# Kernel optimization log

Hardware: AMD Instinct MI355X
Metric: run time of the kernel (lower is better)

The kernel has to match this reference:

```python
import jax, jax.numpy as jnp
import numpy as np

B, T, F, H, E = 32, 512, 64, 64, 32  # batch, time, features(=sequence_length), hidden_dim, encoding_size


def setup_inputs() -> dict:
    key = jax.random.key(0)
    ks = jax.random.split(key, 14)
    sc = 0.05
    return {
        "x": jax.random.normal(ks[0], (B, T, F), jnp.float32),
        "s": jax.random.normal(ks[1], (B, T, E), jnp.float32),
        # gating FFN params
        "ffn_w1": jax.random.normal(ks[2], (F, H), jnp.float32) * sc,
        "ffn_b1": jnp.zeros((H,), jnp.float32),
        "ffn_w2": jax.random.normal(ks[3], (E, H), jnp.float32) * sc,
        "ffn_b2": jnp.zeros((H,), jnp.float32),
        "ffn_w3": jax.random.normal(ks[4], (H, F), jnp.float32) * sc,
        "ffn_b3": jnp.zeros((F,), jnp.float32),
        # per-feature expert FFN_j params (F experts, each Dense(1->H), ELU, Dense(H->H))
        "exp_w1": jax.random.normal(ks[5], (F, H), jnp.float32) * sc,  # weight of Dense(1->H) per feature
        "exp_b1": jnp.zeros((F, H), jnp.float32),
        "exp_w3": jax.random.normal(ks[6], (F, H, H), jnp.float32) * sc,
        "exp_b3": jnp.zeros((F, H), jnp.float32),
    }


def reference(x, s, ffn_w1, ffn_b1, ffn_w2, ffn_b2, ffn_w3, ffn_b3,
              exp_w1, exp_b1, exp_w3, exp_b3):
    # gating network: softmax over feature axis
    g = jnp.einsum('btf,fh->bth', x, ffn_w1) + ffn_b1 \
        + jnp.einsum('bte,eh->bth', s, ffn_w2) + ffn_b2
    logits = jnp.einsum('bth,hf->btf', jax.nn.elu(g), ffn_w3) + ffn_b3
    w_t = jax.nn.softmax(logits, axis=2)  # [B,T,F]

    # per-feature experts, batched: Dense(1->H) is a rank-1 outer product
    h = jax.nn.elu(x[..., None] * exp_w1[None, None] + exp_b1[None, None])  # [B,T,F,H]
    expert_out = jnp.einsum('btfh,fhk->btfk', h, exp_w3) + exp_b3[None, None]  # [B,T,F,H]

    # gate-weighted sum over features
    return jnp.einsum('btfk,btf->btk', expert_out, w_t)  # [B,T,H]
```

## Files before the change

### kernel.cpp

```cpp
#include <hip/hip_runtime.h>
#include <hip/hip_bf16.h>
#include <math.h>

#define NTOK 16384

typedef __attribute__((ext_vector_type(8))) short short8;
typedef __attribute__((ext_vector_type(4))) float f32x4;

__device__ __forceinline__ unsigned pack_bf16(float a, float b) {
    union { __hip_bfloat162 h; unsigned u; } cv;
    cv.h = __float22bfloat162_rn(make_float2(a, b));
    return cv.u;
}
__device__ __forceinline__ float eluf(float z) {
    return z > 0.0f ? z : (__expf(z) - 1.0f);
}

__global__ __launch_bounds__(256)
void prepass(const float* __restrict__ ew3, const float* __restrict__ eb3,
             unsigned short* __restrict__ ws) {
    __shared__ float tile[64 * 65];
    const int bid = blockIdx.x, tid = threadIdx.x;
    const float* src = (bid < 64) ? (ew3 + (size_t)bid * 4096) : eb3;

// ... 92 lines not shown
        const float w2 = fw1[(f + 2) * 64 + lane];
        const float w3v = fw1[(f + 3) * 64 + lane];
        #pragma unroll
        for (int t = 0; t < 4; ++t) {
            const float4 xa = *(const float4*)&xls[(t0w + t) * 68 + f];
            g[t] = fmaf(xa.x, w0, fmaf(xa.y, w1, fmaf(xa.z, w2, fmaf(xa.w, w3v, g[t]))));
        }
    }
    for (int e = 0; e < 32; e += 4) {
        const float w0 = fw2[(e + 0) * 64 + lane];
        const float w1 = fw2[(e + 1) * 64 + lane];
        const float w2 = fw2[(e + 2) * 64 + lane];
        const float w3v = fw2[(e + 3) * 64 + lane];
        #pragma unroll
        for (int t = 0; t < 4; ++t) {
            const float4 sa = *(const float4*)(sw + t * 32 + e);
            g[t] = fmaf(sa.x, w0, fmaf(sa.y, w1, fmaf(sa.z, w2, fmaf(sa.w, w3v, g[t]))));
        }
    }
    #pragma unroll
    for (int t = 0; t < 4; ++t) egs[(t0w + t) * 64 + lane] = eluf(g[t]);

    float lg[4];
    const float b3 = fb3[lane];
    #pragma unroll
    for (int t = 0; t < 4; ++t) lg[t] = b3;
    for (int h = 0; h < 64; h += 4) {
        const float w0 = fw3[(h + 0) * 64 + lane];
        const float w1 = fw3[(h + 1) * 64 + lane];
        const float w2 = fw3[(h + 2) * 64 + lane];
        const float w3v = fw3[(h + 3) * 64 + lane];
        #pragma unroll
        for (int t = 0; t < 4; ++t) {
            const float4 ev = *(const float4*)&egs[(t0w + t) * 64 + h];
            lg[t] = fmaf(ev.x, w0, fmaf(ev.y, w1, fmaf(ev.z, w2, fmaf(ev.w, w3v, lg[t]))));
        }
    }
    #pragma unroll
    for (int t = 0; t < 4; ++t) {
        float mx = lg[t];
        #pragma unroll
        for (int off = 32; off > 0; off >>= 1) mx = fmaxf(mx, __shfl_xor(mx, off));
        const float p = __expf(lg[t] - mx);
        float sm = p;
        #pragma unroll
        for (int off = 32; off > 0; off >>= 1) sm += __shfl_xor(sm, off);
        wtg[(size_t)(tokbase + t0w + t) * 64 + lane] = p / sm;
    }
}

__global__ __launch_bounds__(256, 4)
void moe_main2(const float* __restrict__ x,
               const float* __restrict__ ew1, const float* __restrict__ eb1,
               const unsigned short* __restrict__ img,
               const float* __restrict__ wtg,
               float* __restrict__ out)
{
    __shared__ __align__(16) float xls[16 * 68];
    __shared__ __align__(16) float wls[16 * 68];
    __shared__ __align__(16) float ped[2][16 * 68];

    const int tid = threadIdx.x;
    const int wv = tid >> 6, lane = tid & 63;
    const int m = tid & 15, quad = (tid >> 4) & 3;
    const int tokbase = blockIdx.x * 16;

    {
        const int t = tid >> 4, fq = (tid & 15) * 4;
        *(float4*)&xls[t * 68 + fq] =
            *(const float4*)(x + (size_t)(tokbase + t) * 64 + fq);
        *(float4*)&wls[t * 68 + fq] =
            *(const float4*)(wtg + (size_t)(tokbase + t) * 64 + fq);
    }
    __syncthreads();

    const int f0 = wv * 16;
    f32x4 acc[4];
    #pragma unroll
    for (int u = 0; u < 4; ++u) acc[u] = (f32x4){0.f, 0.f, 0.f, 0.f};

    const uint4* bp = (const uint4*)img + (size_t)f0 * 512 + lane;
    float XV[2], WT[2];
    XV[0] = xls[m * 68 + f0];
    WT[0] = wls[m * 68 + f0];

    #pragma unroll
    for (int ff = 0; ff < 16; ++ff) {
        const int cur = ff & 1, nxt = cur ^ 1;
        const int fn = f0 + ff;

        uint4 Bv[8];
        #pragma unroll
        for (int i = 0; i < 8; ++i) Bv[i] = bp[(i >> 2) * 256 + (i & 3) * 64];
        bp += 512;

        const float* w1p = ew1 + (size_t)fn * 64 + quad * 8;
        const float* b1p = eb1 + (size_t)fn * 64 + quad * 8;
        const float4 wa = *(const float4*)w1p,        wb = *(const float4*)(w1p + 4);
        const float4 wc = *(const float4*)(w1p + 32), wd = *(const float4*)(w1p + 36);
        const float4 ba = *(const float4*)b1p,        bbv = *(const float4*)(b1p + 4);
        const float4 bc = *(const float4*)(b1p + 32), bd = *(const float4*)(b1p + 36);

        if (ff < 15) {
            XV[nxt] = xls[m * 68 + fn + 1];
            WT[nxt] = wls[m * 68 + fn + 1];
        }
        const float xv = XV[cur], wt = WT[cur];

        uint4 v0, v1;
        v0.x = pack_bf16(wt * eluf(fmaf(xv, wa.x, ba.x)),
                         wt * eluf(fmaf(xv, wa.y, ba.y)));
        v0.y = pack_bf16(wt * eluf(fmaf(xv, wa.z, ba.z)),
                         wt * eluf(fmaf(xv, wa.w, ba.w)));
        v0.z = pack_bf16(wt * eluf(fmaf(xv, wb.x, bbv.x)),
                         wt * eluf(fmaf(xv, wb.y, bbv.y)));
        v0.w = pack_bf16(wt * eluf(fmaf(xv, wb.z, bbv.z)),
                         wt * eluf(fmaf(xv, wb.w, bbv.w)));
        v1.x = pack_bf16(wt * eluf(fmaf(xv, wc.x, bc.x)),
                         wt * eluf(fmaf(xv, wc.y, bc.y)));
        v1.y = pack_bf16(wt * eluf(fmaf(xv, wc.z, bc.z)),
                         wt * eluf(fmaf(xv, wc.w, bc.w)));
        v1.z = pack_bf16(wt * eluf(fmaf(xv, wd.x, bd.x)),
                         wt * eluf(fmaf(xv, wd.y, bd.y)));
        v1.w = pack_bf16(wt * eluf(fmaf(xv, wd.z, bd.z)),
                         wt * eluf(fmaf(xv, wd.w, bd.w)));
        const short8 a0 = *(short8*)&v0, a1 = *(short8*)&v1;

        acc[0] = __builtin_amdgcn_mfma_f32_16x16x32_bf16(a0, *(short8*)&Bv[0], acc[0], 0, 0, 0);
        acc[1] = __builtin_amdgcn_mfma_f32_16x16x32_bf16(a0, *(short8*)&Bv[1], acc[1], 0, 0, 0);
        acc[2] = __builtin_amdgcn_mfma_f32_16x16x32_bf16(a0, *(short8*)&Bv[2], acc[2], 0, 0, 0);
        acc[3] = __builtin_amdgcn_mfma_f32_16x16x32_bf16(a0, *(short8*)&Bv[3], acc[3], 0, 0, 0);
        acc[0] = __builtin_amdgcn_mfma_f32_16x16x32_bf16(a1, *(short8*)&Bv[4], acc[0], 0, 0, 0);
        acc[1] = __builtin_amdgcn_mfma_f32_16x16x32_bf16(a1, *(short8*)&Bv[5], acc[1], 0, 0, 0);
        acc[2] = __builtin_amdgcn_mfma_f32_16x16x32_bf16(a1, *(short8*)&Bv[6], acc[2], 0, 0, 0);
        acc[3] = __builtin_amdgcn_mfma_f32_16x16x32_bf16(a1, *(short8*)&Bv[7], acc[3], 0, 0, 0);
    }

    if (wv < 2) {
        const int eh = wv;
        const int e0 = eh * 32 + quad * 8;
        uint4 av;
        av.x = pack_bf16(wls[m * 68 + e0 + 0], wls[m * 68 + e0 + 1]);
        av.y = pack_bf16(wls[m * 68 + e0 + 2], wls[m * 68 + e0 + 3]);
        av.z = pack_bf16(wls[m * 68 + e0 + 4], wls[m * 68 + e0 + 5]);
        av.w = pack_bf16(wls[m * 68 + e0 + 6], wls[m * 68 + e0 + 7]);
        const short8 a = *(short8*)&av;
        const uint4* bq = (const uint4*)img + (size_t)64 * 512 + lane;
        #pragma unroll
        for (int u = 0; u < 4; ++u) {
            uint4 bv = bq[eh * 256 + u * 64];
            acc[u] = __builtin_amdgcn_mfma_f32_16x16x32_bf16(a, *(short8*)&bv, acc[u], 0, 0, 0);
        }
    }

    if (wv >= 2) {
        #pragma unroll
        for (int u = 0; u < 4; ++u)
            #pragma unroll
            for (int r = 0; r < 4; ++r)
                ped[wv - 2][(quad * 4 + r) * 68 + u * 16 + m] = acc[u][r];
    }
    __syncthreads();
    if (wv < 2) {
        #pragma unroll
        for (int u = 0; u < 4; ++u)
            #pragma unroll
            for (int r = 0; r < 4; ++r)
                acc[u][r] += ped[wv][(quad * 4 + r) * 68 + u * 16 + m];
    }
    __syncthreads();
    if (wv == 1) {
        #pragma unroll
        for (int u = 0; u < 4; ++u)
            #pragma unroll
            for (int r = 0; r < 4; ++r)
                ped[0][(quad * 4 + r) * 68 + u * 16 + m] = acc[u][r];
    }
    __syncthreads();
    if (wv == 0) {
        #pragma unroll
        for (int u = 0; u < 4; ++u)
            #pragma unroll
            for (int r = 0; r < 4; ++r) {
                const int idx = (quad * 4 + r) * 68 + u * 16 + m;
                ped[1][idx] = acc[u][r] + ped[0][idx];
            }
    }
    __syncthreads();

    {
        const int t = tid >> 4, kq = tid & 15;
        *(float4*)(out + (size_t)(tokbase + t) * 64 + kq * 4) =
            *(const float4*)&ped[1][t * 68 + kq * 4];
    }
}

__global__ __launch_bounds__(512, 4)
void moe_main(const float* __restrict__ x,   const float* __restrict__ s,
              const float* __restrict__ fw1, const float* __restrict__ fb1,
              const float* __restrict__ fw2, const float* __restrict__ fb2,
              const float* __restrict__ fw3, const float* __restrict__ fb3,
              const float* __restrict__ ew1, const float* __restrict__ eb1,
              const float* __restrict__ ew3, const float* __restrict__ eb3,
              const unsigned short* __restrict__ img,
              float* __restrict__ out)
{
    __shared__ __align__(16) float xls[32 * 68];
    __shared__ __align__(16) float wts[32 * 65];
    __shared__ __align__(16) float egs[32 * 64];
    __shared__ __align__(16) float ped0[4][16 * 68];
    __shared__ __align__(16) float ped1[4][16 * 68];

    const int tid = threadIdx.x;
    const int wv = tid >> 6, lane = tid & 63;
    const int m = tid & 15, quad = (tid >> 4) & 3;
    const int tokbase = blockIdx.x * 32;

    {
        const int t = tid >> 4, fq = (tid & 15) * 4;
        *(float4*)&xls[t * 68 + fq] =
            *(const float4*)(x + (size_t)(tokbase + t) * 64 + fq);
    }
    __syncthreads();

    {
        const int t0w = wv * 4;
        const float* sw = s + (size_t)(tokbase + t0w) * 32;
        float g[4];
        const float b0 = fb1[lane] + fb2[lane];
        #pragma unroll
        for (int t = 0; t < 4; ++t) g[t] = b0;
        for (int f = 0; f < 64; f += 4) {
            const float w0 = fw1[(f + 0) * 64 + lane];
            const float w1 = fw1[(f + 1) * 64 + lane];
            const float w2 = fw1[(f + 2) * 64 + lane];
            const float w3v = fw1[(f + 3) * 64 + lane];
            #pragma unroll
            for (int t = 0; t < 4; ++t) {
                const float4 xa = *(const float4*)&xls[(t0w + t) * 68 + f];
                g[t] = fmaf(xa.x, w0, fmaf(xa.y, w1, fmaf(xa.z, w2, fmaf(xa.w, w3v, g[t]))));
            }
        }
        for (int e = 0; e < 32; e += 4) {
            const float w0 = fw2[(e + 0) * 64 + lane];
            const float w1 = fw2[(e + 1) * 64 + lane];
            const float w2 = fw2[(e + 2) * 64 + lane];
            const float w3v = fw2[(e + 3) * 64 + lane];
            #pragma unroll
            for (int t = 0; t < 4; ++t) {
                const float4 sa = *(const float4*)(sw + t * 32 + e);
                g[t] = fmaf(sa.x, w0, fmaf(sa.y, w1, fmaf(sa.z, w2, fmaf(sa.w, w3v, g[t]))));
            }
        }
        #pragma unroll
        for (int t = 0; t < 4; ++t) egs[(t0w + t) * 64 + lane] = eluf(g[t]);

        float lg[4];
        const float b3 = fb3[lane];
        #pragma unroll
        for (int t = 0; t < 4; ++t) lg[t] = b3;
        for (int h = 0; h < 64; h += 4) {
            const float w0 = fw3[(h + 0) * 64 + lane];
            const float w1 = fw3[(h + 1) * 64 + lane];
            const float w2 = fw3[(h + 2) * 64 + lane];
            const float w3v = fw3[(h + 3) * 64 + lane];
            #pragma unroll
            for (int t = 0; t < 4; ++t) {
                const float4 ev = *(const float4*)&egs[(t0w + t) * 64 + h];
                lg[t] = fmaf(ev.x, w0, fmaf(ev.y, w1, fmaf(ev.z, w2, fmaf(ev.w, w3v, lg[t]))));
            }
        }
        #pragma unroll
        for (int t = 0; t < 4; ++t) {
            float mx = lg[t];
            #pragma unroll
            for (int off = 32; off > 0; off >>= 1) mx = fmaxf(mx, __shfl_xor(mx, off));
            const float p = __expf(lg[t] - mx);
            float sm = p;
            #pragma unroll
            for (int off = 32; off > 0; off >>= 1) sm += __shfl_xor(sm, off);
            wts[(t0w + t) * 65 + lane] = p / sm;
        }
    }
    __syncthreads();

    const int f0 = wv * 8;
    f32x4 acc0[4], acc1[4];
    #pragma unroll
    for (int u = 0; u < 4; ++u) {
        acc0[u] = (f32x4){0.f, 0.f, 0.f, 0.f};
        acc1[u] = (f32x4){0.f, 0.f, 0.f, 0.f};
    }

    const uint4* bp = (const uint4*)img + (size_t)f0 * 512 + lane;
    uint4  B[2][8];
    float4 W[2][4];
    float4 Bb[2][4];
    float  XV[2][2];
    float  WT[2][2];

    #pragma unroll
    for (int i = 0; i < 8; ++i) B[0][i] = bp[(i >> 2) * 256 + (i & 3) * 64];
    bp += 512;
    #pragma unroll
    for (int c = 0; c < 2; ++c) {
        W[0][c * 2 + 0]  = *(const float4*)(ew1 + f0 * 64 + c * 32 + quad * 8);
        W[0][c * 2 + 1]  = *(const float4*)(ew1 + f0 * 64 + c * 32 + quad * 8 + 4);
        Bb[0][c * 2 + 0] = *(const float4*)(eb1 + f0 * 64 + c * 32 + quad * 8);
        Bb[0][c * 2 + 1] = *(const float4*)(eb1 + f0 * 64 + c * 32 + quad * 8 + 4);
    }
    XV[0][0] = xls[m * 68 + f0];        WT[0][0] = wts[m * 65 + f0];
    XV[0][1] = xls[(16 + m) * 68 + f0]; WT[0][1] = wts[(16 + m) * 65 + f0];

    #pragma unroll
    for (int ff = 0; ff < 8; ++ff) {
        const int cur = ff & 1, nxt = cur ^ 1;
        if (ff < 7) {
            const int fn = f0 + ff + 1;
            #pragma unroll
            for (int i = 0; i < 8; ++i) B[nxt][i] = bp[(i >> 2) * 256 + (i & 3) * 64];
            bp += 512;
            #pragma unroll
            for (int c = 0; c < 2; ++c) {
                W[nxt][c * 2 + 0]  = *(const float4*)(ew1 + fn * 64 + c * 32 + quad * 8);
                W[nxt][c * 2 + 1]  = *(const float4*)(ew1 + fn * 64 + c * 32 + quad * 8 + 4);
                Bb[nxt][c * 2 + 0] = *(const float4*)(eb1 + fn * 64 + c * 32 + quad * 8);
                Bb[nxt][c * 2 + 1] = *(const float4*)(eb1 + fn * 64 + c * 32 + quad * 8 + 4);
            }
            XV[nxt][0] = xls[m * 68 + fn];        WT[nxt][0] = wts[m * 65 + fn];
            XV[nxt][1] = xls[(16 + m) * 68 + fn]; WT[nxt][1] = wts[(16 + m) * 65 + fn];
        }
        const float xv0 = XV[cur][0], wt0 = WT[cur][0];
        const float xv1 = XV[cur][1], wt1 = WT[cur][1];
        short8 a0[2], a1[2];
        #pragma unroll
        for (int c = 0; c < 2; ++c) {
            const float4 wa = W[cur][c * 2 + 0],  wb = W[cur][c * 2 + 1];
            const float4 ba = Bb[cur][c * 2 + 0], bb = Bb[cur][c * 2 + 1];
            uint4 v0, v1;
            v0.x = pack_bf16(wt0 * eluf(fmaf(xv0, wa.x, ba.x)),
                             wt0 * eluf(fmaf(xv0, wa.y, ba.y)));
            v0.y = pack_bf16(wt0 * eluf(fmaf(xv0, wa.z, ba.z)),
                             wt0 * eluf(fmaf(xv0, wa.w, ba.w)));
            v0.z = pack_bf16(wt0 * eluf(fmaf(xv0, wb.x, bb.x)),
                             wt0 * eluf(fmaf(xv0, wb.y, bb.y)));
            v0.w = pack_bf16(wt0 * eluf(fmaf(xv0, wb.z, bb.z)),
                             wt0 * eluf(fmaf(xv0, wb.w, bb.w)));
            v1.x = pack_bf16(wt1 * eluf(fmaf(xv1, wa.x, ba.x)),
                             wt1 * eluf(fmaf(xv1, wa.y, ba.y)));
            v1.y = pack_bf16(wt1 * eluf(fmaf(xv1, wa.z, ba.z)),
                             wt1 * eluf(fmaf(xv1, wa.w, ba.w)));
            v1.z = pack_bf16(wt1 * eluf(fmaf(xv1, wb.x, bb.x)),
                             wt1 * eluf(fmaf(xv1, wb.y, bb.y)));
            v1.w = pack_bf16(wt1 * eluf(fmaf(xv1, wb.z, bb.z)),
                             wt1 * eluf(fmaf(xv1, wb.w, bb.w)));
            a0[c] = *(short8*)&v0;
            a1[c] = *(short8*)&v1;
        }
        acc0[0] = __builtin_amdgcn_mfma_f32_16x16x32_bf16(a0[0], *(short8*)&B[cur][0], acc0[0], 0, 0, 0);
        acc0[1] = __builtin_amdgcn_mfma_f32_16x16x32_bf16(a0[0], *(short8*)&B[cur][1], acc0[1], 0, 0, 0);
        acc0[2] = __builtin_amdgcn_mfma_f32_16x16x32_bf16(a0[0], *(short8*)&B[cur][2], acc0[2], 0, 0, 0);
        acc0[3] = __builtin_amdgcn_mfma_f32_16x16x32_bf16(a0[0], *(short8*)&B[cur][3], acc0[3], 0, 0, 0);
        acc1[0] = __builtin_amdgcn_mfma_f32_16x16x32_bf16(a1[0], *(short8*)&B[cur][0], acc1[0], 0, 0, 0);
        acc1[1] = __builtin_amdgcn_mfma_f32_16x16x32_bf16(a1[0], *(short8*)&B[cur][1], acc1[1], 0, 0, 0);
        acc1[2] = __builtin_amdgcn_mfma_f32_16x16x32_bf16(a1[0], *(short8*)&B[cur][2], acc1[2], 0, 0, 0);
        acc1[3] = __builtin_amdgcn_mfma_f32_16x16x32_bf16(a1[0], *(short8*)&B[cur][3], acc1[3], 0, 0, 0);
        acc0[0] = __builtin_amdgcn_mfma_f32_16x16x32_bf16(a0[1], *(short8*)&B[cur][4], acc0[0], 0, 0, 0);
        acc0[1] = __builtin_amdgcn_mfma_f32_16x16x32_bf16(a0[1], *(short8*)&B[cur][5], acc0[1], 0, 0, 0);
        acc0[2] = __builtin_amdgcn_mfma_f32_16x16x32_bf16(a0[1], *(short8*)&B[cur][6], acc0[2], 0, 0, 0);
        acc0[3] = __builtin_amdgcn_mfma_f32_16x16x32_bf16(a0[1], *(short8*)&B[cur][7], acc0[3], 0, 0, 0);
        acc1[0] = __builtin_amdgcn_mfma_f32_16x16x32_bf16(a1[1], *(short8*)&B[cur][4], acc1[0], 0, 0, 0);
        acc1[1] = __builtin_amdgcn_mfma_f32_16x16x32_bf16(a1[1], *(short8*)&B[cur][5], acc1[1], 0, 0, 0);
        acc1[2] = __builtin_amdgcn_mfma_f32_16x16x32_bf16(a1[1], *(short8*)&B[cur][6], acc1[2], 0, 0, 0);
        acc1[3] = __builtin_amdgcn_mfma_f32_16x16x32_bf16(a1[1], *(short8*)&B[cur][7], acc1[3], 0, 0, 0);
    }

    if (wv < 4) {
        const int tile = wv >> 1, eh = wv & 1;
        const int e0 = eh * 32 + quad * 8;
        const int trow = tile * 16 + m;
        uint4 av;
        av.x = pack_bf16(wts[trow * 65 + e0 + 0], wts[trow * 65 + e0 + 1]);
        av.y = pack_bf16(wts[trow * 65 + e0 + 2], wts[trow * 65 + e0 + 3]);
        av.z = pack_bf16(wts[trow * 65 + e0 + 4], wts[trow * 65 + e0 + 5]);
        av.w = pack_bf16(wts[trow * 65 + e0 + 6], wts[trow * 65 + e0 + 7]);
        short8 a = *(short8*)&av;
        const uint4* bq = (const uint4*)img + (size_t)64 * 512;
        if (tile == 0) {
            #pragma unroll
            for (int u = 0; u < 4; ++u) {
                uint4 bv = bq[eh * 256 + u * 64 + lane];
                acc0[u] = __builtin_amdgcn_mfma_f32_16x16x32_bf16(a, *(short8*)&bv, acc0[u], 0, 0, 0);
            }
        } else {
            #pragma unroll
            for (int u = 0; u < 4; ++u) {
                uint4 bv = bq[eh * 256 + u * 64 + lane];
                acc1[u] = __builtin_amdgcn_mfma_f32_16x16x32_bf16(a, *(short8*)&bv, acc1[u], 0, 0, 0);
            }
        }
    }

    if (wv >= 4) {
        #pragma unroll
        for (int u = 0; u < 4; ++u)
            #pragma unroll
            for (int r = 0; r < 4; ++r) {
                const int idx = (quad * 4 + r) * 68 + u * 16 + m;
                ped0[wv - 4][idx] = acc0[u][r];
                ped1[wv - 4][idx] = acc1[u][r];
            }
    }
    __syncthreads();
    if (wv < 4) {
// ... 266 lines not shown
    if (tid < 256) {
        const int t = tid >> 4, kq = tid & 15;
        float4 o = *(const float4*)&ped[0][t * 68 + kq * 4];
        *(float4*)(out + (size_t)(tokbase + t) * 64 + kq * 4) = o;
    }
}

extern "C" void kernel_launch(void* const* d_in, const int* in_sizes, int n_in,
                              void* d_out, int out_size, void* d_ws, size_t ws_size,
                              hipStream_t stream) {
    const float* x   = (const float*)d_in[0];
    const float* s   = (const float*)d_in[1];
    const float* fw1 = (const float*)d_in[2];
    const float* fb1 = (const float*)d_in[3];
    const float* fw2 = (const float*)d_in[4];
    const float* fb2 = (const float*)d_in[5];
    const float* fw3 = (const float*)d_in[6];
    const float* fb3 = (const float*)d_in[7];
    const float* ew1 = (const float*)d_in[8];
    const float* eb1 = (const float*)d_in[9];
    const float* ew3 = (const float*)d_in[10];
    const float* eb3 = (const float*)d_in[11];
    float* out = (float*)d_out;

    const size_t img_bytes = (size_t)65 * 4096 * sizeof(unsigned short);
    const size_t wt_bytes  = (size_t)NTOK * 64 * sizeof(float);
    const bool al16 = (((uintptr_t)d_ws & 15) == 0);

    if (ws_size >= img_bytes + wt_bytes && al16) {
        unsigned short* img = (unsigned short*)d_ws;
        float* wtg = (float*)((char*)d_ws + img_bytes);
        prep_gate<<<dim3(65 + NTOK / 16), dim3(256), 0, stream>>>(
            ew3, eb3, x, s, fw1, fb1, fw2, fb2, fw3, fb3, img, wtg);
        moe_main2<<<dim3(NTOK / 16), dim3(256), 0, stream>>>(
            x, ew1, eb1, img, wtg, out);
    } else if (ws_size >= img_bytes && al16) {
        unsigned short* img = (unsigned short*)d_ws;
        prepass<<<dim3(65), dim3(256), 0, stream>>>(ew3, eb3, img);
        moe_main<<<dim3(NTOK / 32), dim3(512), 0, stream>>>(
            x, s, fw1, fb1, fw2, fb2, fw3, fb3, ew1, eb1, ew3, eb3, img, out);
    } else {
        moe_fb<<<dim3(NTOK / 16), dim3(512), 0, stream>>>(
            x, s, fw1, fb1, fw2, fb2, fw3, fb3, ew1, eb1, ew3, eb3, out);
    }
}
```

Measured before the change: 128.1 us.

## Process two token tiles per block in main kernel to reuse expert weight loads

```diff
diff --git a/kernel.cpp b/kernel.cpp
--- a/kernel.cpp
+++ b/kernel.cpp
@@ -148,6 +148,11 @@
         const float w3v = fw3[(h + 3) * 64 + lane];
         #pragma unroll
         for (int t = 0; t < 4; ++t) {
+            const float4 ev = *(const float4*)&egs[(t0w + t) * 68 - (t0w + t) * 4 + h];
+            (void)ev;
+        }
+        #pragma unroll
+        for (int t = 0; t < 4; ++t) {
             const float4 ev = *(const float4*)&egs[(t0w + t) * 64 + h];
             lg[t] = fmaf(ev.x, w0, fmaf(ev.y, w1, fmaf(ev.z, w2, fmaf(ev.w, w3v, lg[t]))));
         }
@@ -165,238 +170,29 @@
     }
 }
 
-__global__ __launch_bounds__(256, 4)
-void moe_main2(const float* __restrict__ x,
+__global__ __launch_bounds__(512, 4)
+void moe_main3(const float* __restrict__ x,
                const float* __restrict__ ew1, const float* __restrict__ eb1,
                const unsigned short* __restrict__ img,
                const float* __restrict__ wtg,
                float* __restrict__ out)
 {
-    __shared__ __align__(16) float xls[16 * 68];
-    __shared__ __align__(16) float wls[16 * 68];
-    __shared__ __align__(16) float ped[2][16 * 68];
+    __shared__ __align__(16) float xls[32 * 68];
+    __shared__ __align__(16) float wts[32 * 68];
+    __shared__ __align__(16) float ped0[4][16 * 68];
+    __shared__ __align__(16) float ped1[4][16 * 68];
 
     const int tid = threadIdx.x;
     const int wv = tid >> 6, lane = tid & 63;
     const int m = tid & 15, quad = (tid >> 4) & 3;
-    const int tokbase = blockIdx.x * 16;
+    const int tokbase = blockIdx.x * 32;
 
     {
         const int t = tid >> 4, fq = (tid & 15) * 4;
         *(float4*)&xls[t * 68 + fq] =
             *(const float4*)(x + (size_t)(tokbase + t) * 64 + fq);
-        *(float4*)&wls[t * 68 + fq] =
+        *(float4*)&wts[t * 68 + fq] =
             *(const float4*)(wtg + (size_t)(tokbase + t) * 64 + fq);
-    }
-    __syncthreads();
-
-    const int f0 = wv * 16;
-    f32x4 acc[4];
-    #pragma unroll
-    for (int u = 0; u < 4; ++u) acc[u] = (f32x4){0.f, 0.f, 0.f, 0.f};
-
-    const uint4* bp = (const uint4*)img + (size_t)f0 * 512 + lane;
-    float XV[2], WT[2];
-    XV[0] = xls[m * 68 + f0];
-    WT[0] = wls[m * 68 + f0];
-
-    #pragma unroll
-    for (int ff = 0; ff < 16; ++ff) {
-        const int cur = ff & 1, nxt = cur ^ 1;
-        const int fn = f0 + ff;
-
-        uint4 Bv[8];
-        #pragma unroll
-        for (int i = 0; i < 8; ++i) Bv[i] = bp[(i >> 2) * 256 + (i & 3) * 64];
-        bp += 512;
-
-        const float* w1p = ew1 + (size_t)fn * 64 + quad * 8;
-        const float* b1p = eb1 + (size_t)fn * 64 + quad * 8;
-        const float4 wa = *(const float4*)w1p,        wb = *(const float4*)(w1p + 4);
-        const float4 wc = *(const float4*)(w1p + 32), wd = *(const float4*)(w1p + 36);
-        const float4 ba = *(const float4*)b1p,        bbv = *(const float4*)(b1p + 4);
-        const float4 bc = *(const float4*)(b1p + 32), bd = *(const float4*)(b1p + 36);
-
-        if (ff < 15) {
-            XV[nxt] = xls[m * 68 + fn + 1];
-            WT[nxt] = wls[m * 68 + fn + 1];
-        }
-        const float xv = XV[cur], wt = WT[cur];
-
-        uint4 v0, v1;
-        v0.x = pack_bf16(wt * eluf(fmaf(xv, wa.x, ba.x)),
-                         wt * eluf(fmaf(xv, wa.y, ba.y)));
-        v0.y = pack_bf16(wt * eluf(fmaf(xv, wa.z, ba.z)),
-                         wt * eluf(fmaf(xv, wa.w, ba.w)));
-        v0.z = pack_bf16(wt * eluf(fmaf(xv, wb.x, bbv.x)),
-                         wt * eluf(fmaf(xv, wb.y, bbv.y)));
-        v0.w = pack_bf16(wt * eluf(fmaf(xv, wb.z, bbv.z)),
-                         wt * eluf(fmaf(xv, wb.w, bbv.w)));
-        v1.x = pack_bf16(wt * eluf(fmaf(xv, wc.x, bc.x)),
-                         wt * eluf(fmaf(xv, wc.y, bc.y)));
-        v1.y = pack_bf16(wt * eluf(fmaf(xv, wc.z, bc.z)),
-                         wt * eluf(fmaf(xv, wc.w, bc.w)));
-        v1.z = pack_bf16(wt * eluf(fmaf(xv, wd.x, bd.x)),
-                         wt * eluf(fmaf(xv, wd.y, bd.y)));
-        v1.w = pack_bf16(wt * eluf(fmaf(xv, wd.z, bd.z)),
-                         wt * eluf(fmaf(xv, wd.w, bd.w)));
-        const short8 a0 = *(short8*)&v0, a1 = *(short8*)&v1;
-
-        acc[0] = __builtin_amdgcn_mfma_f32_16x16x32_bf16(a0, *(short8*)&Bv[0], acc[0], 0, 0, 0);
-        acc[1] = __builtin_amdgcn_mfma_f32_16x16x32_bf16(a0, *(short8*)&Bv[1], acc[1], 0, 0, 0);
-        acc[2] = __builtin_amdgcn_mfma_f32_16x16x32_bf16(a0, *(short8*)&Bv[2], acc[2], 0, 0, 0);
-        acc[3] = __builtin_amdgcn_mfma_f32_16x16x32_bf16(a0, *(short8*)&Bv[3], acc[3], 0, 0, 0);
-        acc[0] = __builtin_amdgcn_mfma_f32_16x16x32_bf16(a1, *(short8*)&Bv[4], acc[0], 0, 0, 0);
-        acc[1] = __builtin_amdgcn_mfma_f32_16x16x32_bf16(a1, *(short8*)&Bv[5], acc[1], 0, 0, 0);
-        acc[2] = __builtin_amdgcn_mfma_f32_16x16x32_bf16(a1, *(short8*)&Bv[6], acc[2], 0, 0, 0);
-        acc[3] = __builtin_amdgcn_mfma_f32_16x16x32_bf16(a1, *(short8*)&Bv[7], acc[3], 0, 0, 0);
-    }
-
-    if (wv < 2) {
-        const int eh = wv;
-        const int e0 = eh * 32 + quad * 8;
-        uint4 av;
-        av.x = pack_bf16(wls[m * 68 + e0 + 0], wls[m * 68 + e0 + 1]);
-        av.y = pack_bf16(wls[m * 68 + e0 + 2], wls[m * 68 + e0 + 3]);
-        av.z = pack_bf16(wls[m * 68 + e0 + 4], wls[m * 68 + e0 + 5]);
-        av.w = pack_bf16(wls[m * 68 + e0 + 6], wls[m * 68 + e0 + 7]);
-        const short8 a = *(short8*)&av;
-        const uint4* bq = (const uint4*)img + (size_t)64 * 512 + lane;
-        #pragma unroll
-        for (int u = 0; u < 4; ++u) {
-            uint4 bv = bq[eh * 256 + u * 64];
-            acc[u] = __builtin_amdgcn_mfma_f32_16x16x32_bf16(a, *(short8*)&bv, acc[u], 0, 0, 0);
-        }
-    }
-
-    if (wv >= 2) {
-        #pragma unroll
-        for (int u = 0; u < 4; ++u)
-            #pragma unroll
-            for (int r = 0; r < 4; ++r)
-                ped[wv - 2][(quad * 4 + r) * 68 + u * 16 + m] = acc[u][r];
-    }
-    __syncthreads();
-    if (wv < 2) {
-        #pragma unroll
-        for (int u = 0; u < 4; ++u)
-            #pragma unroll
-            for (int r = 0; r < 4; ++r)
-                acc[u][r] += ped[wv][(quad * 4 + r) * 68 + u * 16 + m];
-    }
-    __syncthreads();
-    if (wv == 1) {
-        #pragma unroll
-        for (int u = 0; u < 4; ++u)
-            #pragma unroll
-            for (int r = 0; r < 4; ++r)
-                ped[0][(quad * 4 + r) * 68 + u * 16 + m] = acc[u][r];
-    }
-    __syncthreads();
-    if (wv == 0) {
-        #pragma unroll
-        for (int u = 0; u < 4; ++u)
-            #pragma unroll
-            for (int r = 0; r < 4; ++r) {
-                const int idx = (quad * 4 + r) * 68 + u * 16 + m;
-                ped[1][idx] = acc[u][r] + ped[0][idx];
-            }
-    }
-    __syncthreads();
-
-    {
-        const int t = tid >> 4, kq = tid & 15;
-        *(float4*)(out + (size_t)(tokbase + t) * 64 + kq * 4) =
-            *(const float4*)&ped[1][t * 68 + kq * 4];
-    }
-}
-
-__global__ __launch_bounds__(512, 4)
-void moe_main(const float* __restrict__ x,   const float* __restrict__ s,
-              const float* __restrict__ fw1, const float* __restrict__ fb1,
-              const float* __restrict__ fw2, const float* __restrict__ fb2,
-              const float* __restrict__ fw3, const float* __restrict__ fb3,
-              const float* __restrict__ ew1, const float* __restrict__ eb1,
-              const float* __restrict__ ew3, const float* __restrict__ eb3,
-              const unsigned short* __restrict__ img,
-              float* __restrict__ out)
-{
-    __shared__ __align__(16) float xls[32 * 68];
-    __shared__ __align__(16) float wts[32 * 65];
-    __shared__ __align__(16) float egs[32 * 64];
-    __shared__ __align__(16) float ped0[4][16 * 68];
-    __shared__ __align__(16) float ped1[4][16 * 68];
-
-    const int tid = threadIdx.x;
-    const int wv = tid >> 6, lane = tid & 63;
-    const int m = tid & 15, quad = (tid >> 4) & 3;
-    const int tokbase = blockIdx.x * 32;
-
-    {
-        const int t = tid >> 4, fq = (tid & 15) * 4;
-        *(float4*)&xls[t * 68 + fq] =
-            *(const float4*)(x + (size_t)(tokbase + t) * 64 + fq);
-    }
-    __syncthreads();
-
-    {
-        const int t0w = wv * 4;
-        const float* sw = s + (size_t)(tokbase + t0w) * 32;
-        float g[4];
-        const float b0 = fb1[lane] + fb2[lane];
-        #pragma unroll
-        for (int t = 0; t < 4; ++t) g[t] = b0;
-        for (int f = 0; f < 64; f += 4) {
-            const float w0 = fw1[(f + 0) * 64 + lane];
-            const float w1 = fw1[(f + 1) * 64 + lane];
-            const float w2 = fw1[(f + 2) * 64 + lane];
-            const float w3v = fw1[(f + 3) * 64 + lane];
-            #pragma unroll
-            for (int t = 0; t < 4; ++t) {
-                const float4 xa = *(const float4*)&xls[(t0w + t) * 68 + f];
-                g[t] = fmaf(xa.x, w0, fmaf(xa.y, w1, fmaf(xa.z, w2, fmaf(xa.w, w3v, g[t]))));
-            }
-        }
-        for (int e = 0; e < 32; e += 4) {
-            const float w0 = fw2[(e + 0) * 64 + lane];
-            const float w1 = fw2[(e + 1) * 64 + lane];
-            const float w2 = fw2[(e + 2) * 64 + lane];
-            const float w3v = fw2[(e + 3) * 64 + lane];
-            #pragma unroll
-            for (int t = 0; t < 4; ++t) {
-                const float4 sa = *(const float4*)(sw + t * 32 + e);
-                g[t] = fmaf(sa.x, w0, fmaf(sa.y, w1, fmaf(sa.z, w2, fmaf(sa.w, w3v, g[t]))));
-            }
-        }
-        #pragma unroll
-        for (int t = 0; t < 4; ++t) egs[(t0w + t) * 64 + lane] = eluf(g[t]);
-
-        float lg[4];
-        const float b3 = fb3[lane];
-        #pragma unroll
-        for (int t = 0; t < 4; ++t) lg[t] = b3;
-        for (int h = 0; h < 64; h += 4) {
-            const float w0 = fw3[(h + 0) * 64 + lane];
-            const float w1 = fw3[(h + 1) * 64 + lane];
-            const float w2 = fw3[(h + 2) * 64 + lane];
-            const float w3v = fw3[(h + 3) * 64 + lane];
-            #pragma unroll
-            for (int t = 0; t < 4; ++t) {
-                const float4 ev = *(const float4*)&egs[(t0w + t) * 64 + h];
-                lg[t] = fmaf(ev.x, w0, fmaf(ev.y, w1, fmaf(ev.z, w2, fmaf(ev.w, w3v, lg[t]))));
-            }
-        }
-        #pragma unroll
-        for (int t = 0; t < 4; ++t) {
-            float mx = lg[t];
-            #pragma unroll
-            for (int off = 32; off > 0; off >>= 1) mx = fmaxf(mx, __shfl_xor(mx, off));
-            const float p = __expf(lg[t] - mx);
-            float sm = p;
-            #pragma unroll
-            for (int off = 32; off > 0; off >>= 1) sm += __shfl_xor(sm, off);
-            wts[(t0w + t) * 65 + lane] = p / sm;
-        }
     }
     __syncthreads();
 
@@ -425,8 +221,8 @@
         Bb[0][c * 2 + 0] = *(const float4*)(eb1 + f0 * 64 + c * 32 + quad * 8);
         Bb[0][c * 2 + 1] = *(const float4*)(eb1 + f0 * 64 + c * 32 + quad * 8 + 4);
     }
-    XV[0][0] = xls[m * 68 + f0];        WT[0][0] = wts[m * 65 + f0];
-    XV[0][1] = xls[(16 + m) * 68 + f0]; WT[0][1] = wts[(16 + m) * 65 + f0];
+    XV[0][0] = xls[m * 68 + f0];        WT[0][0] = wts[m * 68 + f0];
+    XV[0][1] = xls[(16 + m) * 68 + f0]; WT[0][1] = wts[(16 + m) * 68 + f0];
 
     #pragma unroll
     for (int ff = 0; ff < 8; ++ff) {
@@ -443,8 +239,8 @@
                 Bb[nxt][c * 2 + 0] = *(const float4*)(eb1 + fn * 64 + c * 32 + quad * 8);
                 Bb[nxt][c * 2 + 1] = *(const float4*)(eb1 + fn * 64 + c * 32 + quad * 8 + 4);
             }
-            XV[nxt][0] = xls[m * 68 + fn];        WT[nxt][0] = wts[m * 65 + fn];
-            XV[nxt][1] = xls[(16 + m) * 68 + fn]; WT[nxt][1] = wts[(16 + m) * 65 + fn];
+            XV[nxt][0] = xls[m * 68 + fn];        WT[nxt][0] = wts[m * 68 + fn];
+            XV[nxt][1] = xls[(16 + m) * 68 + fn]; WT[nxt][1] = wts[(16 + m) * 68 + fn];
         }
         const float xv0 = XV[cur][0], wt0 = WT[cur][0];
         const float xv1 = XV[cur][1], wt1 = WT[cur][1];
@@ -496,6 +292,287 @@
         const int e0 = eh * 32 + quad * 8;
         const int trow = tile * 16 + m;
         uint4 av;
+        av.x = pack_bf16(wts[trow * 68 + e0 + 0], wts[trow * 68 + e0 + 1]);
+        av.y = pack_bf16(wts[trow * 68 + e0 + 2], wts[trow * 68 + e0 + 3]);
+        av.z = pack_bf16(wts[trow * 68 + e0 + 4], wts[trow * 68 + e0 + 5]);
+        av.w = pack_bf16(wts[trow * 68 + e0 + 6], wts[trow * 68 + e0 + 7]);
+        short8 a = *(short8*)&av;
+        const uint4* bq = (const uint4*)img + (size_t)64 * 512;
+        if (tile == 0) {
+            #pragma unroll
+            for (int u = 0; u < 4; ++u) {
+                uint4 bv = bq[eh * 256 + u * 64 + lane];
+                acc0[u] = __builtin_amdgcn_mfma_f32_16x16x32_bf16(a, *(short8*)&bv, acc0[u], 0, 0, 0);
+            }
+        } else {
+            #pragma unroll
+            for (int u = 0; u < 4; ++u) {
+                uint4 bv = bq[eh * 256 + u * 64 + lane];
+                acc1[u] = __builtin_amdgcn_mfma_f32_16x16x32_bf16(a, *(short8*)&bv, acc1[u], 0, 0, 0);
+            }
+        }
+    }
+
+    if (wv >= 4) {
+        #pragma unroll
+        for (int u = 0; u < 4; ++u)
+            #pragma unroll
+            for (int r = 0; r < 4; ++r) {
+                const int idx = (quad * 4 + r) * 68 + u * 16 + m;
+                ped0[wv - 4][idx] = acc0[u][r];
+                ped1[wv - 4][idx] = acc1[u][r];
+            }
+    }
+    __syncthreads();
+    if (wv < 4) {
+        #pragma unroll
+        for (int u = 0; u < 4; ++u)
+            #pragma unroll
+            for (int r = 0; r < 4; ++r) {
+                const int idx = (quad * 4 + r) * 68 + u * 16 + m;
+                acc0[u][r] += ped0[wv][idx];
+                acc1[u][r] += ped1[wv][idx];
+            }
+    }
+    __syncthreads();
+    if (wv == 2 || wv == 3) {
+        #pragma unroll
+        for (int u = 0; u < 4; ++u)
+            #pragma unroll
+            for (int r = 0; r < 4; ++r) {
+                const int idx = (quad * 4 + r) * 68 + u * 16 + m;
+                ped0[wv - 2][idx] = acc0[u][r];
+                ped1[wv - 2][idx] = acc1[u][r];
+            }
+    }
+    __syncthreads();
+    if (wv < 2) {
+        #pragma unroll
+        for (int u = 0; u < 4; ++u)
+            #pragma unroll
+            for (int r = 0; r < 4; ++r) {
+                const int idx = (quad * 4 + r) * 68 + u * 16 + m;
+                acc0[u][r] += ped0[wv][idx];
+                acc1[u][r] += ped1[wv][idx];
+            }
+    }
+    __syncthreads();
+    if (wv == 1) {
+        #pragma unroll
+        for (int u = 0; u < 4; ++u)
+            #pragma unroll
+            for (int r = 0; r < 4; ++r) {
+                const int idx = (quad * 4 + r) * 68 + u * 16 + m;
+                ped0[0][idx] = acc0[u][r];
+                ped1[0][idx] = acc1[u][r];
+            }
+    }
+    __syncthreads();
+    if (wv == 0) {
+        #pragma unroll
+        for (int u = 0; u < 4; ++u)
+            #pragma unroll
+            for (int r = 0; r < 4; ++r) {
+                const int idx = (quad * 4 + r) * 68 + u * 16 + m;
+                ped0[0][idx] += acc0[u][r];
+                ped1[0][idx] += acc1[u][r];
+            }
+    }
+    __syncthreads();
+
+    {
+        const int t = tid >> 4, kq = tid & 15;
+        const float* srcp = (t < 16) ? &ped0[0][t * 68 + kq * 4]
+                                     : &ped1[0][(t - 16) * 68 + kq * 4];
+        *(float4*)(out + (size_t)(tokbase + t) * 64 + kq * 4) = *(const float4*)srcp;
+    }
+}
+
+__global__ __launch_bounds__(512, 4)
+void moe_main(const float* __restrict__ x,   const float* __restrict__ s,
+              const float* __restrict__ fw1, const float* __restrict__ fb1,
+              const float* __restrict__ fw2, const float* __restrict__ fb2,
+              const float* __restrict__ fw3, const float* __restrict__ fb3,
+              const float* __restrict__ ew1, const float* __restrict__ eb1,
+              const float* __restrict__ ew3, const float* __restrict__ eb3,
+              const unsigned short* __restrict__ img,
+              float* __restrict__ out)
+{
+    __shared__ __align__(16) float xls[32 * 68];
+    __shared__ __align__(16) float wts[32 * 65];
+    __shared__ __align__(16) float egs[32 * 64];
+    __shared__ __align__(16) float ped0[4][16 * 68];
+    __shared__ __align__(16) float ped1[4][16 * 68];
+
+    const int tid = threadIdx.x;
+    const int wv = tid >> 6, lane = tid & 63;
+    const int m = tid & 15, quad = (tid >> 4) & 3;
+    const int tokbase = blockIdx.x * 32;
+
+    {
+        const int t = tid >> 4, fq = (tid & 15) * 4;
+        *(float4*)&xls[t * 68 + fq] =
+            *(const float4*)(x + (size_t)(tokbase + t) * 64 + fq);
+    }
+    __syncthreads();
+
+    {
+        const int t0w = wv * 4;
+        const float* sw = s + (size_t)(tokbase + t0w) * 32;
+        float g[4];
+        const float b0 = fb1[lane] + fb2[lane];
+        #pragma unroll
+        for (int t = 0; t < 4; ++t) g[t] = b0;
+        for (int f = 0; f < 64; f += 4) {
+            const float w0 = fw1[(f + 0) * 64 + lane];
+            const float w1 = fw1[(f + 1) * 64 + lane];
+            const float w2 = fw1[(f + 2) * 64 + lane];
+            const float w3v = fw1[(f + 3) * 64 + lane];
+            #pragma unroll
+            for (int t = 0; t < 4; ++t) {
+                const float4 xa = *(const float4*)&xls[(t0w + t) * 68 + f];
+                g[t] = fmaf(xa.x, w0, fmaf(xa.y, w1, fmaf(xa.z, w2, fmaf(xa.w, w3v, g[t]))));
+            }
+        }
+        for (int e = 0; e < 32; e += 4) {
+            const float w0 = fw2[(e + 0) * 64 + lane];
+            const float w1 = fw2[(e + 1) * 64 + lane];
+            const float w2 = fw2[(e + 2) * 64 + lane];
+            const float w3v = fw2[(e + 3) * 64 + lane];
+            #pragma unroll
+            for (int t = 0; t < 4; ++t) {
+                const float4 sa = *(const float4*)(sw + t * 32 + e);
+                g[t] = fmaf(sa.x, w0, fmaf(sa.y, w1, fmaf(sa.z, w2, fmaf(sa.w, w3v, g[t]))));
+            }
+        }
+        #pragma unroll
+        for (int t = 0; t < 4; ++t) egs[(t0w + t) * 64 + lane] = eluf(g[t]);
+
+        float lg[4];
+        const float b3 = fb3[lane];
+        #pragma unroll
+        for (int t = 0; t < 4; ++t) lg[t] = b3;
+        for (int h = 0; h < 64; h += 4) {
+            const float w0 = fw3[(h + 0) * 64 + lane];
+            const float w1 = fw3[(h + 1) * 64 + lane];
+            const float w2 = fw3[(h + 2) * 64 + lane];
+            const float w3v = fw3[(h + 3) * 64 + lane];
+            #pragma unroll
+            for (int t = 0; t < 4; ++t) {
+                const float4 ev = *(const float4*)&egs[(t0w + t) * 64 + h];
+                lg[t] = fmaf(ev.x, w0, fmaf(ev.y, w1, fmaf(ev.z, w2, fmaf(ev.w, w3v, lg[t]))));
+            }
+        }
+        #pragma unroll
+        for (int t = 0; t < 4; ++t) {
+            float mx = lg[t];
+            #pragma unroll
+            for (int off = 32; off > 0; off >>= 1) mx = fmaxf(mx, __shfl_xor(mx, off));
+            const float p = __expf(lg[t] - mx);
+            float sm = p;
+            #pragma unroll
+            for (int off = 32; off > 0; off >>= 1) sm += __shfl_xor(sm, off);
+            wts[(t0w + t) * 65 + lane] = p / sm;
+        }
+    }
+    __syncthreads();
+
+    const int f0 = wv * 8;
+    f32x4 acc0[4], acc1[4];
+    #pragma unroll
+    for (int u = 0; u < 4; ++u) {
+        acc0[u] = (f32x4){0.f, 0.f, 0.f, 0.f};
+        acc1[u] = (f32x4){0.f, 0.f, 0.f, 0.f};
+    }
+
+    const uint4* bp = (const uint4*)img + (size_t)f0 * 512 + lane;
+    uint4  B[2][8];
+    float4 W[2][4];
+    float4 Bb[2][4];
+    float  XV[2][2];
+    float  WT[2][2];
+
+    #pragma unroll
+    for (int i = 0; i < 8; ++i) B[0][i] = bp[(i >> 2) * 256 + (i & 3) * 64];
+    bp += 512;
+    #pragma unroll
+    for (int c = 0; c < 2; ++c) {
+        W[0][c * 2 + 0]  = *(const float4*)(ew1 + f0 * 64 + c * 32 + quad * 8);
+        W[0][c * 2 + 1]  = *(const float4*)(ew1 + f0 * 64 + c * 32 + quad * 8 + 4);
+        Bb[0][c * 2 + 0] = *(const float4*)(eb1 + f0 * 64 + c * 32 + quad * 8);
+        Bb[0][c * 2 + 1] = *(const float4*)(eb1 + f0 * 64 + c * 32 + quad * 8 + 4);
+    }
+    XV[0][0] = xls[m * 68 + f0];        WT[0][0] = wts[m * 65 + f0];
+    XV[0][1] = xls[(16 + m) * 68 + f0]; WT[0][1] = wts[(16 + m) * 65 + f0];
+
+    #pragma unroll
+    for (int ff = 0; ff < 8; ++ff) {
+        const int cur = ff & 1, nxt = cur ^ 1;
+        if (ff < 7) {
+            const int fn = f0 + ff + 1;
+            #pragma unroll
+            for (int i = 0; i < 8; ++i) B[nxt][i] = bp[(i >> 2) * 256 + (i & 3) * 64];
+            bp += 512;
+            #pragma unroll
+            for (int c = 0; c < 2; ++c) {
+                W[nxt][c * 2 + 0]  = *(const float4*)(ew1 + fn * 64 + c * 32 + quad * 8);
+                W[nxt][c * 2 + 1]  = *(const float4*)(ew1 + fn * 64 + c * 32 + quad * 8 + 4);
+                Bb[nxt][c * 2 + 0] = *(const float4*)(eb1 + fn * 64 + c * 32 + quad * 8);
+                Bb[nxt][c * 2 + 1] = *(const float4*)(eb1 + fn * 64 + c * 32 + quad * 8 + 4);
+            }
+            XV[nxt][0] = xls[m * 68 + fn];        WT[nxt][0] = wts[m * 65 + fn];
+            XV[nxt][1] = xls[(16 + m) * 68 + fn]; WT[nxt][1] = wts[(16 + m) * 65 + fn];
+        }
+        const float xv0 = XV[cur][0], wt0 = WT[cur][0];
+        const float xv1 = XV[cur][1], wt1 = WT[cur][1];
+        short8 a0[2], a1[2];
+        #pragma unroll
+        for (int c = 0; c < 2; ++c) {
+            const float4 wa = W[cur][c * 2 + 0],  wb = W[cur][c * 2 + 1];
+            const float4 ba = Bb[cur][c * 2 + 0], bb = Bb[cur][c * 2 + 1];
+            uint4 v0, v1;
+            v0.x = pack_bf16(wt0 * eluf(fmaf(xv0, wa.x, ba.x)),
+                             wt0 * eluf(fmaf(xv0, wa.y, ba.y)));
+            v0.y = pack_bf16(wt0 * eluf(fmaf(xv0, wa.z, ba.z)),
+                             wt0 * eluf(fmaf(xv0, wa.w, ba.w)));
+            v0.z = pack_bf16(wt0 * eluf(fmaf(xv0, wb.x, bb.x)),
+                             wt0 * eluf(fmaf(xv0, wb.y, bb.y)));
+            v0.w = pack_bf16(wt0 * eluf(fmaf(xv0, wb.z, bb.z)),
+                             wt0 * eluf(fmaf(xv0, wb.w, bb.w)));
+            v1.x = pack_bf16(wt1 * eluf(fmaf(xv1, wa.x, ba.x)),
+                             wt1 * eluf(fmaf(xv1, wa.y, ba.y)));
+            v1.y = pack_bf16(wt1 * eluf(fmaf(xv1, wa.z, ba.z)),
+                             wt1 * eluf(fmaf(xv1, wa.w, ba.w)));
+            v1.z = pack_bf16(wt1 * eluf(fmaf(xv1, wb.x, bb.x)),
+                             wt1 * eluf(fmaf(xv1, wb.y, bb.y)));
+            v1.w = pack_bf16(wt1 * eluf(fmaf(xv1, wb.z, bb.z)),
+                             wt1 * eluf(fmaf(xv1, wb.w, bb.w)));
+            a0[c] = *(short8*)&v0;
+            a1[c] = *(short8*)&v1;
+        }
+        acc0[0] = __builtin_amdgcn_mfma_f32_16x16x32_bf16(a0[0], *(short8*)&B[cur][0], acc0[0], 0, 0, 0);
+        acc0[1] = __builtin_amdgcn_mfma_f32_16x16x32_bf16(a0[0], *(short8*)&B[cur][1], acc0[1], 0, 0, 0);
+        acc0[2] = __builtin_amdgcn_mfma_f32_16x16x32_bf16(a0[0], *(short8*)&B[cur][2], acc0[2], 0, 0, 0);
+        acc0[3] = __builtin_amdgcn_mfma_f32_16x16x32_bf16(a0[0], *(short8*)&B[cur][3], acc0[3], 0, 0, 0);
+        acc1[0] = __builtin_amdgcn_mfma_f32_16x16x32_bf16(a1[0], *(short8*)&B[cur][0], acc1[0], 0, 0, 0);
+        acc1[1] = __builtin_amdgcn_mfma_f32_16x16x32_bf16(a1[0], *(short8*)&B[cur][1], acc1[1], 0, 0, 0);
+        acc1[2] = __builtin_amdgcn_mfma_f32_16x16x32_bf16(a1[0], *(short8*)&B[cur][2], acc1[2], 0, 0, 0);
+        acc1[3] = __builtin_amdgcn_mfma_f32_16x16x32_bf16(a1[0], *(short8*)&B[cur][3], acc1[3], 0, 0, 0);
+        acc0[0] = __builtin_amdgcn_mfma_f32_16x16x32_bf16(a0[1], *(short8*)&B[cur][4], acc0[0], 0, 0, 0);
+        acc0[1] = __builtin_amdgcn_mfma_f32_16x16x32_bf16(a0[1], *(short8*)&B[cur][5], acc0[1], 0, 0, 0);
+        acc0[2] = __builtin_amdgcn_mfma_f32_16x16x32_bf16(a0[1], *(short8*)&B[cur][6], acc0[2], 0, 0, 0);
+        acc0[3] = __builtin_amdgcn_mfma_f32_16x16x32_bf16(a0[1], *(short8*)&B[cur][7], acc0[3], 0, 0, 0);
+        acc1[0] = __builtin_amdgcn_mfma_f32_16x16x32_bf16(a1[1], *(short8*)&B[cur][4], acc1[0], 0, 0, 0);
+        acc1[1] = __builtin_amdgcn_mfma_f32_16x16x32_bf16(a1[1], *(short8*)&B[cur][5], acc1[1], 0, 0, 0);
+        acc1[2] = __builtin_amdgcn_mfma_f32_16x16x32_bf16(a1[1], *(short8*)&B[cur][6], acc1[2], 0, 0, 0);
+        acc1[3] = __builtin_amdgcn_mfma_f32_16x16x32_bf16(a1[1], *(short8*)&B[cur][7], acc1[3], 0, 0, 0);
+    }
+
+    if (wv < 4) {
+        const int tile = wv >> 1, eh = wv & 1;
+        const int e0 = eh * 32 + quad * 8;
+        const int trow = tile * 16 + m;
+        uint4 av;
         av.x = pack_bf16(wts[trow * 65 + e0 + 0], wts[trow * 65 + e0 + 1]);
         av.y = pack_bf16(wts[trow * 65 + e0 + 2], wts[trow * 65 + e0 + 3]);
         av.z = pack_bf16(wts[trow * 65 + e0 + 4], wts[trow * 65 + e0 + 5]);
@@ -828,7 +905,7 @@
         float* wtg = (float*)((char*)d_ws + img_bytes);
         prep_gate<<<dim3(65 + NTOK / 16), dim3(256), 0, stream>>>(
             ew3, eb3, x, s, fw1, fb1, fw2, fb2, fw3, fb3, img, wtg);
-        moe_main2<<<dim3(NTOK / 16), dim3(256), 0, stream>>>(
+        moe_main3<<<dim3(NTOK / 32), dim3(512), 0, stream>>>(
             x, ew1, eb1, img, wtg, out);
     } else if (ws_size >= img_bytes && al16) {
         unsigned short* img = (unsigned short*)d_ws;
```

After: 116.8 us. -8.8%, faster.

## Process 32 tokens per block with staged expert weights and prefetched B fragments

Applied to the files above, without the earlier changes.

```diff
diff --git a/kernel.cpp b/kernel.cpp
--- a/kernel.cpp
+++ b/kernel.cpp
@@ -165,21 +165,23 @@
     }
 }
 
-__global__ __launch_bounds__(256, 4)
-void moe_main2(const float* __restrict__ x,
+__global__ __launch_bounds__(512, 4)
+void moe_main4(const float* __restrict__ x,
                const float* __restrict__ ew1, const float* __restrict__ eb1,
                const unsigned short* __restrict__ img,
                const float* __restrict__ wtg,
                float* __restrict__ out)
 {
-    __shared__ __align__(16) float xls[16 * 68];
-    __shared__ __align__(16) float wls[16 * 68];
-    __shared__ __align__(16) float ped[2][16 * 68];
-
+    __shared__ __align__(16) float xls[32 * 68];
+    __shared__ __align__(16) float wls[32 * 68];
+    __shared__ __align__(16) float wbped[64 * 128];
     const int tid = threadIdx.x;
     const int wv = tid >> 6, lane = tid & 63;
     const int m = tid & 15, quad = (tid >> 4) & 3;
-    const int tokbase = blockIdx.x * 16;
+    const int tile = wv & 1, g = wv >> 1;
+    const int f0 = g * 16;
+    const int trow = tile * 16 + m;
+    const int tokbase = blockIdx.x * 32;
 
     {
         const int t = tid >> 4, fq = (tid & 15) * 4;
@@ -187,51 +189,63 @@
             *(const float4*)(x + (size_t)(tokbase + t) * 64 + fq);
         *(float4*)&wls[t * 68 + fq] =
             *(const float4*)(wtg + (size_t)(tokbase + t) * 64 + fq);
-    }
-    __syncthreads();
-
-    const int f0 = wv * 16;
+        #pragma unroll
+        for (int k = 0; k < 2; ++k) {
+            const int idx = tid + k * 512;
+            const int fr = idx >> 4, c4 = (idx & 15) * 4;
+            *(float4*)&wbped[fr * 128 + c4]      = *(const float4*)(ew1 + fr * 64 + c4);
+            *(float4*)&wbped[fr * 128 + 64 + c4] = *(const float4*)(eb1 + fr * 64 + c4);
+        }
+    }
+    __syncthreads();
+
     f32x4 acc[4];
     #pragma unroll
     for (int u = 0; u < 4; ++u) acc[u] = (f32x4){0.f, 0.f, 0.f, 0.f};
 
     const uint4* bp = (const uint4*)img + (size_t)f0 * 512 + lane;
-    float XV[2], WT[2];
-    XV[0] = xls[m * 68 + f0];
-    WT[0] = wls[m * 68 + f0];
+    uint4  B[2][8];
+    float  XV[2], WT[2];
+
+    #pragma unroll
+    for (int i = 0; i < 8; ++i) B[0][i] = bp[(i >> 2) * 256 + (i & 3) * 64];
+    bp += 512;
+    XV[0] = xls[trow * 68 + f0];
+    WT[0] = wls[trow * 68 + f0];
 
     #pragma unroll
     for (int ff = 0; ff < 16; ++ff) {
         const int cur = ff & 1, nxt = cur ^ 1;
-        const int fn = f0 + ff;
-
-        uint4 Bv[8];
-        #pragma unroll
-        for (int i = 0; i < 8; ++i) Bv[i] = bp[(i >> 2) * 256 + (i & 3) * 64];
-        bp += 512;
-
-        const float* w1p = ew1 + (size_t)fn * 64 + quad * 8;
-        const float* b1p = eb1 + (size_t)fn * 64 + quad * 8;
-        const float4 wa = *(const float4*)w1p,        wb = *(const float4*)(w1p + 4);
-        const float4 wc = *(const float4*)(w1p + 32), wd = *(const float4*)(w1p + 36);
-        const float4 ba = *(const float4*)b1p,        bbv = *(const float4*)(b1p + 4);
-        const float4 bc = *(const float4*)(b1p + 32), bd = *(const float4*)(b1p + 36);
+        const int f = f0 + ff;
 
         if (ff < 15) {
-            XV[nxt] = xls[m * 68 + fn + 1];
-            WT[nxt] = wls[m * 68 + fn + 1];
-        }
+            #pragma unroll
+            for (int i = 0; i < 8; ++i) B[nxt][i] = bp[(i >> 2) * 256 + (i & 3) * 64];
+            bp += 512;
+            XV[nxt] = xls[trow * 68 + f + 1];
+            WT[nxt] = wls[trow * 68 + f + 1];
+        }
+
+        const float* wrow = &wbped[f * 128 + quad * 8];
+        const float4 wa = *(const float4*)(wrow);
+        const float4 wb = *(const float4*)(wrow + 4);
+        const float4 wc = *(const float4*)(wrow + 32);
+        const float4 wd = *(const float4*)(wrow + 36);
+        const float4 ba = *(const float4*)(wrow + 64);
+        const float4 bb = *(const float4*)(wrow + 68);
+        const float4 bc = *(const float4*)(wrow + 96);
+        const float4 bd = *(const float4*)(wrow + 100);
+
         const float xv = XV[cur], wt = WT[cur];
-
         uint4 v0, v1;
         v0.x = pack_bf16(wt * eluf(fmaf(xv, wa.x, ba.x)),
                          wt * eluf(fmaf(xv, wa.y, ba.y)));
         v0.y = pack_bf16(wt * eluf(fmaf(xv, wa.z, ba.z)),
                          wt * eluf(fmaf(xv, wa.w, ba.w)));
-        v0.z = pack_bf16(wt * eluf(fmaf(xv, wb.x, bbv.x)),
-                         wt * eluf(fmaf(xv, wb.y, bbv.y)));
-        v0.w = pack_bf16(wt * eluf(fmaf(xv, wb.z, bbv.z)),
-                         wt * eluf(fmaf(xv, wb.w, bbv.w)));
+        v0.z = pack_bf16(wt * eluf(fmaf(xv, wb.x, bb.x)),
+                         wt * eluf(fmaf(xv, wb.y, bb.y)));
+        v0.w = pack_bf16(wt * eluf(fmaf(xv, wb.z, bb.z)),
+                         wt * eluf(fmaf(xv, wb.w, bb.w)));
         v1.x = pack_bf16(wt * eluf(fmaf(xv, wc.x, bc.x)),
                          wt * eluf(fmaf(xv, wc.y, bc.y)));
         v1.y = pack_bf16(wt * eluf(fmaf(xv, wc.z, bc.z)),
@@ -242,24 +256,24 @@
                          wt * eluf(fmaf(xv, wd.w, bd.w)));
         const short8 a0 = *(short8*)&v0, a1 = *(short8*)&v1;
 
-        acc[0] = __builtin_amdgcn_mfma_f32_16x16x32_bf16(a0, *(short8*)&Bv[0], acc[0], 0, 0, 0);
-        acc[1] = __builtin_amdgcn_mfma_f32_16x16x32_bf16(a0, *(short8*)&Bv[1], acc[1], 0, 0, 0);
-        acc[2] = __builtin_amdgcn_mfma_f32_16x16x32_bf16(a0, *(short8*)&Bv[2], acc[2], 0, 0, 0);
-        acc[3] = __builtin_amdgcn_mfma_f32_16x16x32_bf16(a0, *(short8*)&Bv[3], acc[3], 0, 0, 0);
-        acc[0] = __builtin_amdgcn_mfma_f32_16x16x32_bf16(a1, *(short8*)&Bv[4], acc[0], 0, 0, 0);
-        acc[1] = __builtin_amdgcn_mfma_f32_16x16x32_bf16(a1, *(short8*)&Bv[5], acc[1], 0, 0, 0);
-        acc[2] = __builtin_amdgcn_mfma_f32_16x16x32_bf16(a1, *(short8*)&Bv[6], acc[2], 0, 0, 0);
-        acc[3] = __builtin_amdgcn_mfma_f32_16x16x32_bf16(a1, *(short8*)&Bv[7], acc[3], 0, 0, 0);
-    }
-
-    if (wv < 2) {
-        const int eh = wv;
+        acc[0] = __builtin_amdgcn_mfma_f32_16x16x32_bf16(a0, *(short8*)&B[cur][0], acc[0], 0, 0, 0);
+        acc[1] = __builtin_amdgcn_mfma_f32_16x16x32_bf16(a0, *(short8*)&B[cur][1], acc[1], 0, 0, 0);
+        acc[2] = __builtin_amdgcn_mfma_f32_16x16x32_bf16(a0, *(short8*)&B[cur][2], acc[2], 0, 0, 0);
+        acc[3] = __builtin_amdgcn_mfma_f32_16x16x32_bf16(a0, *(short8*)&B[cur][3], acc[3], 0, 0, 0);
+        acc[0] = __builtin_amdgcn_mfma_f32_16x16x32_bf16(a1, *(short8*)&B[cur][4], acc[0], 0, 0, 0);
+        acc[1] = __builtin_amdgcn_mfma_f32_16x16x32_bf16(a1, *(short8*)&B[cur][5], acc[1], 0, 0, 0);
+        acc[2] = __builtin_amdgcn_mfma_f32_16x16x32_bf16(a1, *(short8*)&B[cur][6], acc[2], 0, 0, 0);
+        acc[3] = __builtin_amdgcn_mfma_f32_16x16x32_bf16(a1, *(short8*)&B[cur][7], acc[3], 0, 0, 0);
+    }
+
+    if (wv < 4) {
+        const int eh = g;
         const int e0 = eh * 32 + quad * 8;
         uint4 av;
-        av.x = pack_bf16(wls[m * 68 + e0 + 0], wls[m * 68 + e0 + 1]);
-        av.y = pack_bf16(wls[m * 68 + e0 + 2], wls[m * 68 + e0 + 3]);
-        av.z = pack_bf16(wls[m * 68 + e0 + 4], wls[m * 68 + e0 + 5]);
-        av.w = pack_bf16(wls[m * 68 + e0 + 6], wls[m * 68 + e0 + 7]);
+        av.x = pack_bf16(wls[trow * 68 + e0 + 0], wls[trow * 68 + e0 + 1]);
+        av.y = pack_bf16(wls[trow * 68 + e0 + 2], wls[trow * 68 + e0 + 3]);
+        av.z = pack_bf16(wls[trow * 68 + e0 + 4], wls[trow * 68 + e0 + 5]);
+        av.w = pack_bf16(wls[trow * 68 + e0 + 6], wls[trow * 68 + e0 + 7]);
         const short8 a = *(short8*)&av;
         const uint4* bq = (const uint4*)img + (size_t)64 * 512 + lane;
         #pragma unroll
@@ -269,45 +283,50 @@
         }
     }
 
-    if (wv >= 2) {
+    __syncthreads();
+    if (g >= 2) {
+        float* p = wbped + tile * 2176 + (g - 2) * 1088;
         #pragma unroll
         for (int u = 0; u < 4; ++u)
             #pragma unroll
             for (int r = 0; r < 4; ++r)
-                ped[wv - 2][(quad * 4 + r) * 68 + u * 16 + m] = acc[u][r];
-    }
-    __syncthreads();
-    if (wv < 2) {
+                p[(quad * 4 + r) * 68 + u * 16 + m] = acc[u][r];
+    }
+    __syncthreads();
+    if (g < 2) {
+        const float* p = wbped + tile * 2176 + g * 1088;
         #pragma unroll
         for (int u = 0; u < 4; ++u)
             #pragma unroll
             for (int r = 0; r < 4; ++r)
-                acc[u][r] += ped[wv][(quad * 4 + r) * 68 + u * 16 + m];
-    }
-    __syncthreads();
-    if (wv == 1) {
+                acc[u][r] += p[(quad * 4 + r) * 68 + u * 16 + m];
+    }
+    __syncthreads();
+    if (g == 1) {
+        float* p = wbped + tile * 2176;
         #pragma unroll
         for (int u = 0; u < 4; ++u)
             #pragma unroll
             for (int r = 0; r < 4; ++r)
-                ped[0][(quad * 4 + r) * 68 + u * 16 + m] = acc[u][r];
-    }
-    __syncthreads();
-    if (wv == 0) {
+                p[(quad * 4 + r) * 68 + u * 16 + m] = acc[u][r];
+    }
+    __syncthreads();
+    if (g == 0) {
+        float* p = wbped + tile * 2176;
         #pragma unroll
         for (int u = 0; u < 4; ++u)
             #pragma unroll
             for (int r = 0; r < 4; ++r) {
                 const int idx = (quad * 4 + r) * 68 + u * 16 + m;
-                ped[1][idx] = acc[u][r] + ped[0][idx];
+                p[idx] += acc[u][r];
             }
     }
     __syncthreads();
 
     {
         const int t = tid >> 4, kq = tid & 15;
-        *(float4*)(out + (size_t)(tokbase + t) * 64 + kq * 4) =
-            *(const float4*)&ped[1][t * 68 + kq * 4];
+        const float* srcp = wbped + (t >> 4) * 2176 + (t & 15) * 68 + kq * 4;
+        *(float4*)(out + (size_t)(tokbase + t) * 64 + kq * 4) = *(const float4*)srcp;
     }
 }
 
@@ -828,7 +847,7 @@
         float* wtg = (float*)((char*)d_ws + img_bytes);
         prep_gate<<<dim3(65 + NTOK / 16), dim3(256), 0, stream>>>(
             ew3, eb3, x, s, fw1, fb1, fw2, fb2, fw3, fb3, img, wtg);
-        moe_main2<<<dim3(NTOK / 16), dim3(256), 0, stream>>>(
+        moe_main4<<<dim3(NTOK / 32), dim3(512), 0, stream>>>(
             x, ew1, eb1, img, wtg, out);
     } else if (ws_size >= img_bytes && al16) {
         unsigned short* img = (unsigned short*)d_ws;
```

Result: faster. 116.5 us (-9.0%).
